# Optimization experiments

Hardware: AMD Instinct MI355X
Metric: run time of the kernel (lower is better)

The kernel has to match this reference:

```python
import jax, jax.numpy as jnp
import numpy as np

B, N, M, K, D, DO = 4, 32768, 8192, 16, 128, 128


def setup_inputs() -> dict:
    key = jax.random.key(0)
    ks = jax.random.split(key, 8)
    return dict(
        xyz=jax.random.normal(ks[0], (B, N, 3), jnp.float32),
        x=jax.random.normal(ks[1], (B, D, N), jnp.float32),
        xyz_center=jax.random.normal(ks[2], (B, M, 3), jnp.float32),
        idx=jax.random.randint(ks[3], (B, M, K), 0, N, jnp.int32),
        alpha=jnp.ones((1,), jnp.float32),
        beta=jnp.ones((1,), jnp.float32),
        norm_radius=jnp.ones((1,), jnp.float32),
        w1=jax.random.normal(ks[4], (K, 3), jnp.float32) * 0.1,
        g1=jnp.ones((K,), jnp.float32),
        b1=jnp.zeros((K,), jnp.float32),
        w2=jax.random.normal(ks[5], (K, 2 * K), jnp.float32) * 0.1,
        g2=jnp.ones((K,), jnp.float32),
        b2=jnp.zeros((K,), jnp.float32),
        w3=jax.random.normal(ks[6], (K, 2 * K), jnp.float32) * 0.1,
        cv_w=jax.random.normal(ks[7], (DO, D, K), jnp.float32) * 0.02,
    )


def _inorm(t, g, b, eps=1e-5):
    # InstanceNorm2d: normalize each (batch, channel) plane over spatial dims (m, k)
    mu = t.mean(axis=(2, 3), keepdims=True)
    var = t.var(axis=(2, 3), keepdims=True)
    return (t - mu) * jax.lax.rsqrt(var + eps) * g[None, :, None, None] + b[None, :, None, None]


def reference(xyz, x, xyz_center, idx, alpha, beta, norm_radius, w1, g1, b1, w2, g2, b2, w3, cv_w):
    k = idx.shape[-1]
    gather = jax.vmap(lambda pts, i: pts[i])  # per-batch gather
    xyz_group = gather(xyz, idx)                      # b m k 3
    x_group = gather(jnp.swapaxes(x, 1, 2), idx)      # b m k d

    pts = xyz_group - xyz_center[:, :, None, :]       # b m k 3
    # dist computed on detached pts (torch .detach())
    dist = jnp.sqrt(jnp.sum(jnp.square(jax.lax.stop_gradient(pts)), -1))  # b m k
    mean_radius = dist.max(-1).mean()
    nr = norm_radius * 0.9 + mean_radius * 0.1        # EMA-updated radius (non-trainable)
    pts = pts / nr

    dw = jax.nn.sigmoid(-alpha * dist + beta)         # b m k
    s = dw.sum(-1, keepdims=True)
    s = s + (s == 0).astype(dw.dtype) + 1e-6
    dw = dw / s * k
    dw4 = dw[:, None, :, :]                           # b 1 m k

    ptsT = jnp.transpose(pts, (0, 3, 1, 2))           # b 3 m k
    mat = jax.nn.relu(_inorm(jnp.einsum('bcmk,oc->bomk', ptsT, w1), g1, b1))
    mp1 = jnp.broadcast_to((mat * dw4).max(-1, keepdims=True), mat.shape)
    mat = jax.nn.relu(_inorm(jnp.einsum('bcmk,oc->bomk', jnp.concatenate([mat, mp1], 1), w2), g2, b2))
    mp2 = jnp.broadcast_to((mat * dw4).max(-1, keepdims=True), mat.shape)
    mat = jax.nn.relu(jnp.einsum('bcmk,oc->bomk', jnp.concatenate([mat, mp2], 1), w3)) * dw4

    out = jnp.einsum('bmkd,bjmk->bdmj', x_group, mat)  # b d m k
    out = jnp.einsum('bdmj,odj->bom', out, cv_w)
    return out
```

## Files before the change

kernel.cpp:

```cpp
#include <hip/hip_runtime.h>
#include <hip/hip_bf16.h>

#define BB 4
#define NN 32768
#define MM 8192
#define KK 16
#define DD 128
#define DOUT 128
#define TT 2048

typedef unsigned short ushortT;
typedef unsigned int uintT;
typedef __attribute__((ext_vector_type(8))) short short8;
typedef __attribute__((ext_vector_type(4))) float f32x4;

__device__ __forceinline__ ushortT f2bf(float f) {
  union { float f; uintT u; } v; v.f = f;
  uintT u = v.u;
  return (ushortT)((u + 0x7FFFu + ((u >> 16) & 1u)) >> 16);
}

#define ST_MAXD 0
#define ST_E1 16
#define ST_A1 160
#define ST_B1 224
#define ST_E2 288
#define ST_A2 416
#define ST_B2 480

__global__ __launch_bounds__(256) void kxT(const float* __restrict__ x, ushortT* __restrict__ xTb) {
  __shared__ float tile[32][33];
  const int b = blockIdx.z;
  const int n0 = blockIdx.x * 32, d0 = blockIdx.y * 32;
  const int tx = threadIdx.x, ty = threadIdx.y;
  const float* xp = x + (size_t)b * DD * NN;
  #pragma unroll
  for (int i = 0; i < 4; i++)
    tile[ty + i * 8][tx] = xp[(size_t)(d0 + ty + i * 8) * NN + n0 + tx];
  __syncthreads();
  ushortT* op = xTb + (size_t)b * NN * DD;
  #pragma unroll
  for (int i = 0; i < 4; i++)
    op[(size_t)(n0 + ty + i * 8) * DD + d0 + tx] = f2bf(tile[tx][ty + i * 8]);
}

__global__ __launch_bounds__(256) void kWb(const float* __restrict__ cw, ushortT* __restrict__ wb) {
  const int i = blockIdx.x * 256 + threadIdx.x;
  wb[i] = f2bf(cw[i]);
}

__global__ __launch_bounds__(256) void kpassA(const float* __restrict__ xyz,
    const float* __restrict__ xyzc, const int* __restrict__ idx,
    const float* __restrict__ w1, float* __restrict__ st, float4* __restrict__ pts4) {
  const int b = blockIdx.y;
  const int tid = threadIdx.x;
  const int mloc = tid >> 4, k = tid & 15;
  const int m = blockIdx.x * 16 + mloc;
  const int gi = (b * MM + m) * KK + k;
  const int n = idx[gi];
  const float cx = xyzc[(b * MM + m) * 3 + 0];
  const float cy = xyzc[(b * MM + m) * 3 + 1];
  const float cz = xyzc[(b * MM + m) * 3 + 2];
  const float* p = xyz + ((size_t)b * NN + n) * 3;
  const float px = p[0] - cx, py = p[1] - cy, pz = p[2] - cz;
  const float dist = sqrtf(px * px + py * py + pz * pz);
  pts4[gi] = (float4){px, py, pz, dist};
  float maxd = dist;
  maxd = fmaxf(maxd, __shfl_xor(maxd, 1));
  maxd = fmaxf(maxd, __shfl_xor(maxd, 2));
  maxd = fmaxf(maxd, __shfl_xor(maxd, 4));
  maxd = fmaxf(maxd, __shfl_xor(maxd, 8));
  __shared__ float red[16];
  __shared__ float wred[4][32];
  if (k == 0) red[mloc] = maxd;
  float vs[16], vq[16];
  #pragma unroll
  for (int o = 0; o < 16; o++) {
    float e = px * w1[3 * o] + py * w1[3 * o + 1] + pz * w1[3 * o + 2];
    vs[o] = e; vq[o] = e * e;
  }
  #pragma unroll
  for (int s = 1; s < 64; s <<= 1) {
    #pragma unroll
    for (int o = 0; o < 16; o++) {
      vs[o] += __shfl_xor(vs[o], s);
      vq[o] += __shfl_xor(vq[o], s);
    }
  }
  const int wv = tid >> 6, lane = tid & 63;
  if (lane == 0) {
    #pragma unroll
    for (int o = 0; o < 16; o++) { wred[wv][o] = vs[o]; wred[wv][16 + o] = vq[o]; }
  }
  __syncthreads();
  if (tid < 32) {
    float a = wred[0][tid] + wred[1][tid] + wred[2][tid] + wred[3][tid];
    atomicAdd(&st[ST_E1 + b * 32 + tid], a);
  }
  if (tid == 0) {
    float s = 0.f;
    #pragma unroll
    for (int i = 0; i < 16; i++) s += red[i];
    atomicAdd(&st[ST_MAXD], s);
  }
}

__global__ void kS1(const float* __restrict__ nrad, const float* __restrict__ g1,
                    const float* __restrict__ b1, float* __restrict__ st) {
  const int tid = threadIdx.x;
  if (tid >= 64) return;
  const float meanrad = st[ST_MAXD] / (float)(BB * MM);
  const float nr = nrad[0] * 0.9f + meanrad * 0.1f;
  const int b = tid >> 4, o = tid & 15;
  const float cnt = (float)(MM * KK);
  const float sum = st[ST_E1 + b * 32 + o];
  const float sq  = st[ST_E1 + b * 32 + 16 + o];
  const float mu = sum / cnt;
  float var = sq / cnt - mu * mu; var = fmaxf(var, 0.f);
  const float invs = rsqrtf(var + 1e-5f * nr * nr);
  const float a = invs * g1[o];
  st[ST_A1 + b * 16 + o] = a;
  st[ST_B1 + b * 16 + o] = b1[o] - mu * a;
}

__global__ __launch_bounds__(256) void kpassB(const float4* __restrict__ pts4,
    const float* __restrict__ alpha, const float* __restrict__ beta,
    const float* __restrict__ w1, const float* __restrict__ w2,
    float* __restrict__ st) {
  const int b = blockIdx.y;
  const int tid = threadIdx.x;
  __shared__ float w2s[512];
  __shared__ float wred[4][32];
  w2s[tid] = w2[tid]; w2s[256 + tid] = w2[256 + tid];
  const int gi = b * MM * KK + blockIdx.x * 256 + tid;
  const float4 p4 = pts4[gi];
  const float px = p4.x, py = p4.y, pz = p4.z, dist = p4.w;
  float dwv = 1.f / (1.f + expf(alpha[0] * dist - beta[0]));
  float s = dwv;
  s += __shfl_xor(s, 1); s += __shfl_xor(s, 2); s += __shfl_xor(s, 4); s += __shfl_xor(s, 8);
  s = s + (s == 0.f ? 1.f : 0.f) + 1e-6f;
  dwv = dwv / s * 16.f;
  float mat1[16], mp1[16];
  #pragma unroll
  for (int o = 0; o < 16; o++) {
    float e = px * w1[3 * o] + py * w1[3 * o + 1] + pz * w1[3 * o + 2];
    float v = e * st[ST_A1 + b * 16 + o] + st[ST_B1 + b * 16 + o];
    mat1[o] = fmaxf(v, 0.f);
    float t = mat1[o] * dwv;
    t = fmaxf(t, __shfl_xor(t, 1)); t = fmaxf(t, __shfl_xor(t, 2));
    t = fmaxf(t, __shfl_xor(t, 4)); t = fmaxf(t, __shfl_xor(t, 8));
    mp1[o] = t;
  }
  __syncthreads();
  float vs[16], vq[16];
  #pragma unroll
  for (int o = 0; o < 16; o++) {
    float acc = 0.f;
    #pragma unroll
    for (int c = 0; c < 16; c++)
      acc += mat1[c] * w2s[o * 32 + c] + mp1[c] * w2s[o * 32 + 16 + c];
    vs[o] = acc; vq[o] = acc * acc;
  }
  #pragma unroll
  for (int s2 = 1; s2 < 64; s2 <<= 1) {
    #pragma unroll
    for (int o = 0; o < 16; o++) {
      vs[o] += __shfl_xor(vs[o], s2);
      vq[o] += __shfl_xor(vq[o], s2);
    }
  }
  const int wv = tid >> 6, lane = tid & 63;
  if (lane == 0) {
    #pragma unroll
    for (int o = 0; o < 16; o++) { wred[wv][o] = vs[o]; wred[wv][16 + o] = vq[o]; }
  }
  __syncthreads();
  if (tid < 32) {
    float a = wred[0][tid] + wred[1][tid] + wred[2][tid] + wred[3][tid];
    atomicAdd(&st[ST_E2 + b * 32 + tid], a);
  }
}

__global__ void kS2(const float* __restrict__ g2, const float* __restrict__ b2,
                    float* __restrict__ st) {
  const int tid = threadIdx.x;
  if (tid >= 64) return;
  const int b = tid >> 4, o = tid & 15;
  const float cnt = (float)(MM * KK);
  const float sum = st[ST_E2 + b * 32 + o];
  const float sq  = st[ST_E2 + b * 32 + 16 + o];
  const float mu = sum / cnt;
  float var = sq / cnt - mu * mu; var = fmaxf(var, 0.f);
  const float invs = rsqrtf(var + 1e-5f);
  const float a = invs * g2[o];
  st[ST_A2 + b * 16 + o] = a;
  st[ST_B2 + b * 16 + o] = b2[o] - mu * a;
}

__global__ __launch_bounds__(512, 4) void kF1(const float4* __restrict__ pts4,
    const int* __restrict__ idx,
    const float* __restrict__ alpha, const float* __restrict__ beta,
    const float* __restrict__ w1, const float* __restrict__ w2, const float* __restrict__ w3,
    const float* __restrict__ st, const ushortT* __restrict__ xTb, ushortT* __restrict__ Aout) {
  __shared__ float w2s[512], w3s[512];
  __shared__ float mat3s[16 * 320];
  __shared__ int nls[256];
  const int b = blockIdx.y;
  const int tid = threadIdx.x;
  const int m0 = blockIdx.x * 16;
  w2s[tid] = w2[tid];
  w3s[tid] = w3[tid];

  float mat1[16], mp1[16], dwv = 0.f;
  int mloc = 0, k1 = 0;
  if (tid < 256) {
    mloc = tid >> 4; k1 = tid & 15;
    const int gi = (b * MM + m0) * KK + tid;
    nls[tid] = idx[gi];
    const float4 p4 = pts4[gi];
    const float px = p4.x, py = p4.y, pz = p4.z, dist = p4.w;
    dwv = 1.f / (1.f + expf(alpha[0] * dist - beta[0]));
    float s = dwv;
    s += __shfl_xor(s, 1); s += __shfl_xor(s, 2); s += __shfl_xor(s, 4); s += __shfl_xor(s, 8);
    s = s + (s == 0.f ? 1.f : 0.f) + 1e-6f;
    dwv = dwv / s * 16.f;
    #pragma unroll
    for (int o = 0; o < 16; o++) {
      float e = px * w1[3 * o] + py * w1[3 * o + 1] + pz * w1[3 * o + 2];
      float v = e * st[ST_A1 + b * 16 + o] + st[ST_B1 + b * 16 + o];
      mat1[o] = fmaxf(v, 0.f);
      float t = mat1[o] * dwv;
      t = fmaxf(t, __shfl_xor(t, 1)); t = fmaxf(t, __shfl_xor(t, 2));
      t = fmaxf(t, __shfl_xor(t, 4)); t = fmaxf(t, __shfl_xor(t, 8));
      mp1[o] = t;
    }
  }
  __syncthreads();
  if (tid < 256) {
    float mat2[16], mp2[16];
    #pragma unroll
    for (int o = 0; o < 16; o++) {
      float acc = 0.f;
      #pragma unroll
      for (int c = 0; c < 16; c++)
        acc += mat1[c] * w2s[o * 32 + c] + mp1[c] * w2s[o * 32 + 16 + c];
      float v = acc * st[ST_A2 + b * 16 + o] + st[ST_B2 + b * 16 + o];
      mat2[o] = fmaxf(v, 0.f);
      float t = mat2[o] * dwv;
      t = fmaxf(t, __shfl_xor(t, 1)); t = fmaxf(t, __shfl_xor(t, 2));
      t = fmaxf(t, __shfl_xor(t, 4)); t = fmaxf(t, __shfl_xor(t, 8));
      mp2[o] = t;
    }
    float* m3w = &mat3s[mloc * 320 + k1 * 20];
    #pragma unroll
    for (int j = 0; j < 16; j++) {
      float acc = 0.f;
      #pragma unroll
      for (int c = 0; c < 16; c++)
        acc += mat2[c] * w3s[j * 32 + c] + mp2[c] * w3s[j * 32 + 16 + c];
      m3w[j] = fmaxf(acc, 0.f) * dwv;
    }
  }
  __syncthreads();

  const int ml = tid >> 5, dl = tid & 31;
  const int d0 = dl * 4;
  const ushortT* xb = xTb + (size_t)b * NN * DD + d0;
  const float* m3base = &mat3s[ml * 320];
  const int* nbase = &nls[ml * 16];
  float acc[4][16];
  #pragma unroll
  for (int d = 0; d < 4; d++)
    #pragma unroll
    for (int j = 0; j < 16; j++) acc[d][j] = 0.f;
  #pragma unroll 4
  for (int k = 0; k < 16; k++) {
    const int nn = nbase[k];
    const uint2 xv = *(const uint2*)(xb + (size_t)nn * DD);
    float xs[4];
    xs[0] = __uint_as_float(xv.x << 16);
    xs[1] = __uint_as_float(xv.x & 0xFFFF0000u);
    xs[2] = __uint_as_float(xv.y << 16);
    xs[3] = __uint_as_float(xv.y & 0xFFFF0000u);
    const float4 m30 = *(const float4*)(m3base + k * 20 + 0);
    const float4 m31 = *(const float4*)(m3base + k * 20 + 4);
    const float4 m32 = *(const float4*)(m3base + k * 20 + 8);
    const float4 m33 = *(const float4*)(m3base + k * 20 + 12);
    #pragma unroll
    for (int d = 0; d < 4; d++) {
      acc[d][0]  += xs[d] * m30.x; acc[d][1]  += xs[d] * m30.y;
      acc[d][2]  += xs[d] * m30.z; acc[d][3]  += xs[d] * m30.w;
      acc[d][4]  += xs[d] * m31.x; acc[d][5]  += xs[d] * m31.y;
      acc[d][6]  += xs[d] * m31.z; acc[d][7]  += xs[d] * m31.w;
      acc[d][8]  += xs[d] * m32.x; acc[d][9]  += xs[d] * m32.y;
      acc[d][10] += xs[d] * m32.z; acc[d][11] += xs[d] * m32.w;
      acc[d][12] += xs[d] * m33.x; acc[d][13] += xs[d] * m33.y;
      acc[d][14] += xs[d] * m33.z; acc[d][15] += xs[d] * m33.w;
    }
  }
  ushortT* aop = Aout + ((size_t)b * MM + m0 + ml) * TT + d0 * 16;
  #pragma unroll
  for (int d = 0; d < 4; d++) {
    uintT u[8];
    #pragma unroll
    for (int i = 0; i < 8; i++)
      u[i] = (uintT)f2bf(acc[d][2 * i]) | ((uintT)f2bf(acc[d][2 * i + 1]) << 16);
    uint4* dst = (uint4*)(aop + d * 16);
    dst[0] = (uint4){u[0], u[1], u[2], u[3]};
    dst[1] = (uint4){u[4], u[5], u[6], u[7]};
  }
}

__global__ __launch_bounds__(512) void kgemm(const ushortT* __restrict__ Wb,
                                             const ushortT* __restrict__ Aout,
                                             float* __restrict__ out) {
  __shared__ ushortT At[128 * 40];
  __shared__ ushortT Bt[128 * 40];
  const int b = blockIdx.y;
  const int m0 = blockIdx.x * 128;
  const int tid = threadIdx.x;
  const int w = tid >> 6, l = tid & 63;
  const int ow = (w >> 2) * 64, mw = (w & 3) * 32;
  const int fr = l & 15, fg = l >> 4;
  f32x4 acc[4][2];
  #pragma unroll
  for (int i = 0; i < 4; i++)
    #pragma unroll
    for (int j = 0; j < 2; j++)
      acc[i][j] = (f32x4){0.f, 0.f, 0.f, 0.f};
  const int srow = tid >> 2, sk = (tid & 3) * 8;
  const ushortT* wp = Wb + srow * TT + sk;
  const ushortT* ap = Aout + ((size_t)b * MM + m0 + srow) * TT + sk;
  for (int k0 = 0; k0 < TT; k0 += 32) {
    uint4 wv = *(const uint4*)(wp + k0);
    uint4 av = *(const uint4*)(ap + k0);
    *(uint4*)&At[srow * 40 + sk] = wv;
    *(uint4*)&Bt[srow * 40 + sk] = av;
    __syncthreads();
    short8 a[4], bfrag[2];
    #pragma unroll
    for (int i = 0; i < 4; i++) a[i] = *(short8*)&At[(ow + i * 16 + fr) * 40 + fg * 8];
    #pragma unroll
    for (int j = 0; j < 2; j++) bfrag[j] = *(short8*)&Bt[(mw + j * 16 + fr) * 40 + fg * 8];
    #pragma unroll
    for (int i = 0; i < 4; i++)
      #pragma unroll
      for (int j = 0; j < 2; j++)
        acc[i][j] = __builtin_amdgcn_mfma_f32_16x16x32_bf16(a[i], bfrag[j], acc[i][j], 0, 0, 0);
    __syncthreads();
  }
  #pragma unroll
  for (int i = 0; i < 4; i++)
    #pragma unroll
    for (int j = 0; j < 2; j++)
      #pragma unroll
      for (int r = 0; r < 4; r++) {
        const int o = ow + i * 16 + fg * 4 + r;
        const int m = m0 + mw + j * 16 + fr;
        out[((size_t)b * DOUT + o) * MM + m] = acc[i][j][r];
      }
}

#define XTB_OFF 0
#define PTS_OFF 33554432
#define AOUT_OFF 67108864
#define WB_OFF 201326592
#define ST_OFF 201850880

extern "C" void kernel_launch(void* const* d_in, const int* in_sizes, int n_in,
                              void* d_out, int out_size, void* d_ws, size_t ws_size,
                              hipStream_t stream) {
  const float* xyz  = (const float*)d_in[0];
  const float* x    = (const float*)d_in[1];
  const float* xyzc = (const float*)d_in[2];
  const int*   idx  = (const int*)d_in[3];
  const float* alpha = (const float*)d_in[4];
  const float* beta  = (const float*)d_in[5];
  const float* nrad  = (const float*)d_in[6];
  const float* w1 = (const float*)d_in[7];
  const float* g1 = (const float*)d_in[8];
  const float* b1 = (const float*)d_in[9];
  const float* w2 = (const float*)d_in[10];
  const float* g2 = (const float*)d_in[11];
  const float* b2 = (const float*)d_in[12];
  const float* w3 = (const float*)d_in[13];
  const float* cvw = (const float*)d_in[14];
  char* ws = (char*)d_ws;
  ushortT* xTb  = (ushortT*)(ws + XTB_OFF);
  float4*  pts4 = (float4*)(ws + PTS_OFF);
  ushortT* Aout = (ushortT*)(ws + AOUT_OFF);
  ushortT* Wb   = (ushortT*)(ws + WB_OFF);
  float*   st   = (float*)(ws + ST_OFF);
  float* out = (float*)d_out;

  hipMemsetAsync(st, 0, 4096, stream);
  kxT<<<dim3(NN / 32, DD / 32, BB), dim3(32, 8), 0, stream>>>(x, xTb);
  kWb<<<dim3(DOUT * TT / 256), 256, 0, stream>>>(cvw, Wb);
  kpassA<<<dim3(MM / 16, BB), 256, 0, stream>>>(xyz, xyzc, idx, w1, st, pts4);
  kS1<<<1, 64, 0, stream>>>(nrad, g1, b1, st);
  kpassB<<<dim3(MM / 16, BB), 256, 0, stream>>>(pts4, alpha, beta, w1, w2, st);
  kS2<<<1, 64, 0, stream>>>(g2, b2, st);
  kF1<<<dim3(MM / 16, BB), 512, 0, stream>>>(pts4, idx, alpha, beta, w1, w2, w3, st, xTb, Aout);
  kgemm<<<dim3(MM / 128, BB), 512, 0, stream>>>(Wb, Aout, out);
}
```

Baseline: 243.2 us.

## Use all 512 threads for per-point MLP in kF1 and vectorize accumulation as packed float2

kF1 now processes 32 centers per block instead of 16, so all 512 threads compute the per-neighbor MLP stages rather than half of them idling. The gather-accumulate phase loops over two 16-center groups per block. Accumulators become float2 vectors so the compiler can emit packed FMA instructions. This halves the grid size and doubles shared memory for mat3s, which may lower occupancy.

```diff
diff --git a/kernel.cpp b/kernel.cpp
--- a/kernel.cpp
+++ b/kernel.cpp
@@ -13,6 +13,7 @@
 typedef unsigned int uintT;
 typedef __attribute__((ext_vector_type(8))) short short8;
 typedef __attribute__((ext_vector_type(4))) float f32x4;
+typedef __attribute__((ext_vector_type(2))) float f32x2;
 
 __device__ __forceinline__ ushortT f2bf(float f) {
   union { float f; uintT u; } v; v.f = f;
@@ -203,40 +204,39 @@
     const float* __restrict__ w1, const float* __restrict__ w2, const float* __restrict__ w3,
     const float* __restrict__ st, const ushortT* __restrict__ xTb, ushortT* __restrict__ Aout) {
   __shared__ float w2s[512], w3s[512];
-  __shared__ float mat3s[16 * 320];
-  __shared__ int nls[256];
+  __shared__ float mat3s[32 * 320];
+  __shared__ int nls[512];
   const int b = blockIdx.y;
   const int tid = threadIdx.x;
-  const int m0 = blockIdx.x * 16;
+  const int m0 = blockIdx.x * 32;
   w2s[tid] = w2[tid];
   w3s[tid] = w3[tid];
 
-  float mat1[16], mp1[16], dwv = 0.f;
-  int mloc = 0, k1 = 0;
-  if (tid < 256) {
-    mloc = tid >> 4; k1 = tid & 15;
-    const int gi = (b * MM + m0) * KK + tid;
-    nls[tid] = idx[gi];
-    const float4 p4 = pts4[gi];
-    const float px = p4.x, py = p4.y, pz = p4.z, dist = p4.w;
-    dwv = 1.f / (1.f + expf(alpha[0] * dist - beta[0]));
+  const int mloc = tid >> 4, k1 = tid & 15;
+  const int gi = (b * MM + m0) * KK + tid;
+  nls[tid] = idx[gi];
+  const float4 p4 = pts4[gi];
+  const float px = p4.x, py = p4.y, pz = p4.z, dist = p4.w;
+  float dwv = 1.f / (1.f + expf(alpha[0] * dist - beta[0]));
+  {
     float s = dwv;
     s += __shfl_xor(s, 1); s += __shfl_xor(s, 2); s += __shfl_xor(s, 4); s += __shfl_xor(s, 8);
     s = s + (s == 0.f ? 1.f : 0.f) + 1e-6f;
     dwv = dwv / s * 16.f;
-    #pragma unroll
-    for (int o = 0; o < 16; o++) {
-      float e = px * w1[3 * o] + py * w1[3 * o + 1] + pz * w1[3 * o + 2];
-      float v = e * st[ST_A1 + b * 16 + o] + st[ST_B1 + b * 16 + o];
-      mat1[o] = fmaxf(v, 0.f);
-      float t = mat1[o] * dwv;
-      t = fmaxf(t, __shfl_xor(t, 1)); t = fmaxf(t, __shfl_xor(t, 2));
-      t = fmaxf(t, __shfl_xor(t, 4)); t = fmaxf(t, __shfl_xor(t, 8));
-      mp1[o] = t;
-    }
-  }
-  __syncthreads();
-  if (tid < 256) {
+  }
+  float mat1[16], mp1[16];
+  #pragma unroll
+  for (int o = 0; o < 16; o++) {
+    float e = px * w1[3 * o] + py * w1[3 * o + 1] + pz * w1[3 * o + 2];
+    float v = e * st[ST_A1 + b * 16 + o] + st[ST_B1 + b * 16 + o];
+    mat1[o] = fmaxf(v, 0.f);
+    float t = mat1[o] * dwv;
+    t = fmaxf(t, __shfl_xor(t, 1)); t = fmaxf(t, __shfl_xor(t, 2));
+    t = fmaxf(t, __shfl_xor(t, 4)); t = fmaxf(t, __shfl_xor(t, 8));
+    mp1[o] = t;
+  }
+  __syncthreads();
+  {
     float mat2[16], mp2[16];
     #pragma unroll
     for (int o = 0; o < 16; o++) {
@@ -263,51 +263,56 @@
   }
   __syncthreads();
 
-  const int ml = tid >> 5, dl = tid & 31;
+  const int dl = tid & 31;
   const int d0 = dl * 4;
   const ushortT* xb = xTb + (size_t)b * NN * DD + d0;
-  const float* m3base = &mat3s[ml * 320];
-  const int* nbase = &nls[ml * 16];
-  float acc[4][16];
-  #pragma unroll
-  for (int d = 0; d < 4; d++)
-    #pragma unroll
-    for (int j = 0; j < 16; j++) acc[d][j] = 0.f;
-  #pragma unroll 4
-  for (int k = 0; k < 16; k++) {
-    const int nn = nbase[k];
-    const uint2 xv = *(const uint2*)(xb + (size_t)nn * DD);
-    float xs[4];
-    xs[0] = __uint_as_float(xv.x << 16);
-    xs[1] = __uint_as_float(xv.x & 0xFFFF0000u);
-    xs[2] = __uint_as_float(xv.y << 16);
-    xs[3] = __uint_as_float(xv.y & 0xFFFF0000u);
-    const float4 m30 = *(const float4*)(m3base + k * 20 + 0);
-    const float4 m31 = *(const float4*)(m3base + k * 20 + 4);
-    const float4 m32 = *(const float4*)(m3base + k * 20 + 8);
-    const float4 m33 = *(const float4*)(m3base + k * 20 + 12);
+  #pragma unroll 1
+  for (int g = 0; g < 2; g++) {
+    const int ml = g * 16 + (tid >> 5);
+    const float* m3base = &mat3s[ml * 320];
+    const int* nbase = &nls[ml * 16];
+    f32x2 a2[4][8];
+    #pragma unroll
+    for (int d = 0; d < 4; d++)
+      #pragma unroll
+      for (int c = 0; c < 8; c++) a2[d][c] = (f32x2){0.f, 0.f};
+    #pragma unroll 4
+    for (int k = 0; k < 16; k++) {
+      const int nn = nbase[k];
+      const uint2 xv = *(const uint2*)(xb + (size_t)nn * DD);
+      float xs[4];
+      xs[0] = __uint_as_float(xv.x << 16);
+      xs[1] = __uint_as_float(xv.x & 0xFFFF0000u);
+      xs[2] = __uint_as_float(xv.y << 16);
+      xs[3] = __uint_as_float(xv.y & 0xFFFF0000u);
+      const f32x4 m30 = *(const f32x4*)(m3base + k * 20 + 0);
+      const f32x4 m31 = *(const f32x4*)(m3base + k * 20 + 4);
+      const f32x4 m32 = *(const f32x4*)(m3base + k * 20 + 8);
+      const f32x4 m33 = *(const f32x4*)(m3base + k * 20 + 12);
+      f32x2 mp[8];
+      mp[0] = m30.lo; mp[1] = m30.hi;
+      mp[2] = m31.lo; mp[3] = m31.hi;
+      mp[4] = m32.lo; mp[5] = m32.hi;
+      mp[6] = m33.lo; mp[7] = m33.hi;
+      #pragma unroll
+      for (int d = 0; d < 4; d++) {
+        const float xd = xs[d];
+        #pragma unroll
+        for (int c = 0; c < 8; c++)
+          a2[d][c] += mp[c] * xd;
+      }
+    }
+    ushortT* aop = Aout + ((size_t)b * MM + m0 + ml) * TT + d0 * 16;
     #pragma unroll
     for (int d = 0; d < 4; d++) {
-      acc[d][0]  += xs[d] * m30.x; acc[d][1]  += xs[d] * m30.y;
-      acc[d][2]  += xs[d] * m30.z; acc[d][3]  += xs[d] * m30.w;
-      acc[d][4]  += xs[d] * m31.x; acc[d][5]  += xs[d] * m31.y;
-      acc[d][6]  += xs[d] * m31.z; acc[d][7]  += xs[d] * m31.w;
-      acc[d][8]  += xs[d] * m32.x; acc[d][9]  += xs[d] * m32.y;
-      acc[d][10] += xs[d] * m32.z; acc[d][11] += xs[d] * m32.w;
-      acc[d][12] += xs[d] * m33.x; acc[d][13] += xs[d] * m33.y;
-      acc[d][14] += xs[d] * m33.z; acc[d][15] += xs[d] * m33.w;
-    }
-  }
-  ushortT* aop = Aout + ((size_t)b * MM + m0 + ml) * TT + d0 * 16;
-  #pragma unroll
-  for (int d = 0; d < 4; d++) {
-    uintT u[8];
-    #pragma unroll
-    for (int i = 0; i < 8; i++)
-      u[i] = (uintT)f2bf(acc[d][2 * i]) | ((uintT)f2bf(acc[d][2 * i + 1]) << 16);
-    uint4* dst = (uint4*)(aop + d * 16);
-    dst[0] = (uint4){u[0], u[1], u[2], u[3]};
-    dst[1] = (uint4){u[4], u[5], u[6], u[7]};
+      uintT u[8];
+      #pragma unroll
+      for (int i = 0; i < 8; i++)
+        u[i] = (uintT)f2bf(a2[d][i].x) | ((uintT)f2bf(a2[d][i].y) << 16);
+      uint4* dst = (uint4*)(aop + d * 16);
+      dst[0] = (uint4){u[0], u[1], u[2], u[3]};
+      dst[1] = (uint4){u[4], u[5], u[6], u[7]};
+    }
   }
 }
 
@@ -400,6 +405,6 @@
   kS1<<<1, 64, 0, stream>>>(nrad, g1, b1, st);
   kpassB<<<dim3(MM / 16, BB), 256, 0, stream>>>(pts4, alpha, beta, w1, w2, st);
   kS2<<<1, 64, 0, stream>>>(g2, b2, st);
-  kF1<<<dim3(MM / 16, BB), 512, 0, stream>>>(pts4, idx, alpha, beta, w1, w2, w3, st, xTb, Aout);
+  kF1<<<dim3(MM / 32, BB), 512, 0, stream>>>(pts4, idx, alpha, beta, w1, w2, w3, st, xTb, Aout);
   kgemm<<<dim3(MM / 128, BB), 512, 0, stream>>>(Wb, Aout, out);
 }
```

New measurement: 233.9 us. 3.8% less time.
